# Performance work log

Hardware: AMD Instinct MI355X
Metric: run time of the kernel (lower is better)

Reference implementation:

```python
import jax, jax.numpy as jnp
import numpy as np

N = 8192      # nodes (= hidden_channels / heads)
E = 262144    # edges (avg degree 32)
IN = 256      # in_channels
H = 8         # heads
C = 32        # out_channels per head
NEG_SLOPE = 0.2


def setup_inputs() -> dict:
    key = jax.random.key(0)
    ks = jax.random.split(key, 8)
    x = jax.random.normal(ks[0], (N, IN), jnp.float32)
    edge_index = jax.random.randint(ks[1], (2, E), 0, N, dtype=jnp.int32)
    lin_w = jax.random.normal(ks[2], (H * C, IN), jnp.float32) * (1.0 / np.sqrt(IN))
    att_src = jax.random.normal(ks[3], (H, C), jnp.float32) * 0.1
    att_dst = jax.random.normal(ks[4], (H, C), jnp.float32) * 0.1
    bias = jax.random.normal(ks[5], (H * C,), jnp.float32) * 0.01
    out_w = jax.random.normal(ks[6], (C, N * H * C), jnp.float32) * (1.0 / np.sqrt(N * H * C))
    out_b = jax.random.normal(ks[7], (C,), jnp.float32) * 0.01
    return {"x": x, "edge_index": edge_index, "lin_w": lin_w, "att_src": att_src,
            "att_dst": att_dst, "bias": bias, "out_w": out_w, "out_b": out_b}


def reference(x, edge_index, lin_w, att_src, att_dst, bias, out_w, out_b):
    n = x.shape[0]
    # PyG GATConv default: add self loops
    loop = jnp.arange(n, dtype=edge_index.dtype)
    src = jnp.concatenate([edge_index[0], loop])  # message sources j
    dst = jnp.concatenate([edge_index[1], loop])  # message targets i
    # per-head linear projection: [n, H, C]
    xh = (x @ lin_w.T).reshape(n, H, C)
    a_src = jnp.einsum('nhc,hc->nh', xh, att_src)  # [n, H]
    a_dst = jnp.einsum('nhc,hc->nh', xh, att_dst)  # [n, H]
    # edge attention logits + segment softmax over incoming edges of each dst
    e = jax.nn.leaky_relu(a_src[src] + a_dst[dst], negative_slope=NEG_SLOPE)  # [E', H]
    m = jax.ops.segment_max(e, dst, num_segments=n)        # [n, H]
    ex = jnp.exp(e - m[dst])
    denom = jax.ops.segment_sum(ex, dst, num_segments=n)   # [n, H]
    alpha = ex / denom[dst]                                 # [E', H]
    # weighted scatter-add aggregation
    agg = jax.ops.segment_sum(alpha[:, :, None] * xh[src], dst, num_segments=n)  # [n, H, C]
    out = agg.reshape(n, H * C) + bias
    # flatten all nodes, dense output layer, softmax
    y = out.reshape(-1) @ out_w.T + out_b  # [C]
    return jax.nn.softmax(y)
```

## Files before the change

kernel.cpp:

```cpp
#include <hip/hip_runtime.h>


namespace {
constexpr int  kN    = 8192;
constexpr int  kE    = 262144;
constexpr int  kTotE = kE + kN;
constexpr long kK    = 2097152;
constexpr int  kNBF  = 2048;
}

__global__ __launch_bounds__(256) void gemm_xh(const float* __restrict__ x,
                                               const float* __restrict__ lw,
                                               float* __restrict__ xh) {
  __shared__ float As[16][68];
  __shared__ float Bs[16][68];
  const int t  = threadIdx.x;
  const int tx = t & 15, ty = t >> 4;
  const int rowBase = blockIdx.x * 64;
  const int colBase = blockIdx.y * 64;
  const int lr = t >> 2;
  const int lk = (t & 3) * 4;

  float acc[4][4] = {};
  for (int kc = 0; kc < 256; kc += 16) {
    float4 av = *(const float4*)(x  + (long)(rowBase + lr) * 256 + kc + lk);
    float4 bv = *(const float4*)(lw + (long)(colBase + lr) * 256 + kc + lk);
    __syncthreads();
    As[lk + 0][lr] = av.x; As[lk + 1][lr] = av.y; As[lk + 2][lr] = av.z; As[lk + 3][lr] = av.w;
    Bs[lk + 0][lr] = bv.x; Bs[lk + 1][lr] = bv.y; Bs[lk + 2][lr] = bv.z; Bs[lk + 3][lr] = bv.w;
    __syncthreads();
#pragma unroll
    for (int k = 0; k < 16; k++) {
      float4 a4 = *(const float4*)(&As[k][ty * 4]);
      float4 b4 = *(const float4*)(&Bs[k][tx * 4]);
      float aa[4] = {a4.x, a4.y, a4.z, a4.w};
      float bb[4] = {b4.x, b4.y, b4.z, b4.w};
#pragma unroll
      for (int i = 0; i < 4; i++)
#pragma unroll
        for (int j = 0; j < 4; j++) acc[i][j] += aa[i] * bb[j];
    }
  }
#pragma unroll
  for (int i = 0; i < 4; i++) {
    float4 o = make_float4(acc[i][0], acc[i][1], acc[i][2], acc[i][3]);
    *(float4*)(xh + (long)(rowBase + ty * 4 + i) * 256 + colBase + tx * 4) = o;
  }
}

__global__ __launch_bounds__(256) void att_cnt(const float* __restrict__ xh,
                                               const float* __restrict__ att_s,
                                               const float* __restrict__ att_d,
                                               float* __restrict__ a_src,
                                               float* __restrict__ a_dst,
                                               int* __restrict__ cnt) {
  const int n = blockIdx.x, t = threadIdx.x;
  float v = xh[(long)n * 256 + t];
  float s = v * att_s[t];
  float d = v * att_d[t];
#pragma unroll
  for (int off = 16; off; off >>= 1) {
    s += __shfl_down(s, off, 32);
    d += __shfl_down(d, off, 32);
  }
  if ((t & 31) == 0) {
    a_src[n * 8 + (t >> 5)] = s;
    a_dst[n * 8 + (t >> 5)] = d;
  }
  if (t == 0) cnt[n] = 1;
}

__global__ __launch_bounds__(256) void degree(const int* __restrict__ ei, int* __restrict__ cnt) {
  int idx = blockIdx.x * 256 + threadIdx.x;
  if (idx < kE) atomicAdd(&cnt[ei[kE + idx]], 1);
}

__global__ __launch_bounds__(1024) void scan_cnt(const int* __restrict__ cnt,
                                                 int* __restrict__ rowptr,
                                                 int* __restrict__ wpos) {
  __shared__ int s[1024];
  const int t = threadIdx.x;
  int v[8]; int sum = 0;
#pragma unroll
  for (int q = 0; q < 8; q++) { v[q] = cnt[t * 8 + q]; sum += v[q]; }
  s[t] = sum;
  __syncthreads();
  for (int off = 1; off < 1024; off <<= 1) {
    int add = (t >= off) ? s[t - off] : 0;
    __syncthreads();
    s[t] += add;
    __syncthreads();
  }
  int excl = s[t] - sum;
#pragma unroll
  for (int q = 0; q < 8; q++) {
    rowptr[t * 8 + q] = excl;
    wpos[t * 8 + q]   = excl;
    excl += v[q];
  }
  if (t == 1023) rowptr[kN] = s[1023];
}

__global__ __launch_bounds__(256) void scatter_csr(const int* __restrict__ ei,
                                                   const float* __restrict__ a_src,
                                                   const float* __restrict__ a_dst,
                                                   int* __restrict__ wpos,
                                                   int* __restrict__ csr,
                                                   float* __restrict__ w8) {
  int idx = blockIdx.x * 256 + threadIdx.x;
  if (idx >= kTotE) return;
  int s, d;
  if (idx < kE) { s = ei[idx]; d = ei[kE + idx]; }
  else          { s = idx - kE; d = s; }
  int pos = atomicAdd(&wpos[d], 1);
  csr[pos] = s;
  float4 s0 = *(const float4*)(a_src + s * 8);
  float4 s1 = *(const float4*)(a_src + s * 8 + 4);
  float4 d0 = *(const float4*)(a_dst + d * 8);
  float4 d1 = *(const float4*)(a_dst + d * 8 + 4);
  float e[8] = {s0.x + d0.x, s0.y + d0.y, s0.z + d0.z, s0.w + d0.w,
                s1.x + d1.x, s1.y + d1.y, s1.z + d1.z, s1.w + d1.w};
  float w[8];
#pragma unroll
  for (int h = 0; h < 8; h++) {
    float ee = (e[h] > 0.f) ? e[h] : 0.2f * e[h];
    w[h] = __expf(ee);
  }
  float4* wp = (float4*)(w8 + (long)pos * 8);
  wp[0] = make_float4(w[0], w[1], w[2], w[3]);
  wp[1] = make_float4(w[4], w[5], w[6], w[7]);
}

__global__ __launch_bounds__(256) void agg_kernel(const float* __restrict__ xh,
                                                  const float* __restrict__ w8,
                                                  const int* __restrict__ rowptr,
                                                  const int* __restrict__ csr,
                                                  const float* __restrict__ bias,
                                                  float* __restrict__ out_flat) {
  const int i = blockIdx.x, t = threadIdx.x, h = t >> 5;
  const int beg = rowptr[i], end = rowptr[i + 1];
  float acc = 0.f, den = 0.f;
  int j = beg;
  for (; j + 4 <= end; j += 4) {
    int s0 = csr[j], s1 = csr[j + 1], s2 = csr[j + 2], s3 = csr[j + 3];
    float w0 = w8[(long)(j + 0) * 8 + h];
    float w1 = w8[(long)(j + 1) * 8 + h];
    float w2 = w8[(long)(j + 2) * 8 + h];
    float w3 = w8[(long)(j + 3) * 8 + h];
    float f0 = xh[(long)s0 * 256 + t];
    float f1 = xh[(long)s1 * 256 + t];
    float f2 = xh[(long)s2 * 256 + t];
    float f3 = xh[(long)s3 * 256 + t];
    den += (w0 + w1) + (w2 + w3);
    acc += w0 * f0;
    acc += w1 * f1;
    acc += w2 * f2;
    acc += w3 * f3;
  }
  for (; j < end; j++) {
    int s = csr[j];
    float w = w8[(long)j * 8 + h];
    den += w;
    acc += w * xh[(long)s * 256 + t];
  }
  out_flat[(long)i * 256 + t] = acc / den + bias[t];
}

__global__ __launch_bounds__(256) void final_dot(const float* __restrict__ of,
                                                 const float* __restrict__ w,
                                                 float* __restrict__ part) {
  const int t = threadIdx.x, b = blockIdx.x;
  const long k = (long)b * 1024 + t * 4;
  float4 f = *(const float4*)(of + k);
  float acc[32];
#pragma unroll
  for (int c = 0; c < 32; c++) {
    float4 wv = *(const float4*)(w + (long)c * kK + k);
    acc[c] = wv.x * f.x + wv.y * f.y + wv.z * f.z + wv.w * f.w;
  }
#pragma unroll
  for (int c = 0; c < 32; c++) {
    float v = acc[c];
    v += __shfl_down(v, 32, 64);
    v += __shfl_down(v, 16, 64);
    v += __shfl_down(v, 8, 64);
    v += __shfl_down(v, 4, 64);
    v += __shfl_down(v, 2, 64);
    v += __shfl_down(v, 1, 64);
    acc[c] = v;
  }
  __shared__ float s[4][32];
  const int lane = t & 63, wid = t >> 6;
  if (lane == 0) {
#pragma unroll
    for (int c = 0; c < 32; c++) s[wid][c] = acc[c];
  }
  __syncthreads();
  if (t < 32) part[b * 32 + t] = s[0][t] + s[1][t] + s[2][t] + s[3][t];
}

__global__ __launch_bounds__(1024) void finalize(const float* __restrict__ part,
                                                 const float* __restrict__ ob,
                                                 float* __restrict__ out) {
  __shared__ float s[32][33];
  const int t = threadIdx.x;
  const int c = t & 31, r = t >> 5;
  float sum = 0.f;
  for (int i = r; i < kNBF; i += 32) sum += part[i * 32 + c];
  s[c][r] = sum;
  __syncthreads();
  if (t < 32) {
    float y = ob[t];
#pragma unroll
    for (int r2 = 0; r2 < 32; r2++) y += s[t][r2];
    float m = y;
#pragma unroll
    for (int off = 16; off; off >>= 1) m = fmaxf(m, __shfl_xor(m, off, 32));
    float e = __expf(y - m);
    float d = e;
#pragma unroll
    for (int off = 16; off; off >>= 1) d += __shfl_xor(d, off, 32);
    out[t] = e / d;
  }
}

extern "C" void kernel_launch(void* const* d_in, const int* in_sizes, int n_in,
                              void* d_out, int out_size, void* d_ws, size_t ws_size,
                              hipStream_t stream) {
  (void)in_sizes; (void)n_in; (void)out_size; (void)ws_size;
  const float* x     = (const float*)d_in[0];
  const int*   ei    = (const int*)  d_in[1];
  const float* lin_w = (const float*)d_in[2];
  const float* att_s = (const float*)d_in[3];
  const float* att_d = (const float*)d_in[4];
  const float* bias  = (const float*)d_in[5];
  const float* out_w = (const float*)d_in[6];
  const float* out_b = (const float*)d_in[7];
  float* out = (float*)d_out;

  float* xh       = (float*)d_ws;
  float* out_flat = xh + kK;
  float* a_src    = out_flat + kK;
  float* a_dst    = a_src + kN * 8;
  float* part     = a_dst + kN * 8;
  float* w8       = part + (long)kNBF * 32;
  int*   cnt      = (int*)(w8 + (long)kTotE * 8);
  int*   rowptr   = cnt + kN;
  int*   wpos     = rowptr + (kN + 1);
  int*   csr      = wpos + kN;

  gemm_xh    <<<dim3(128, 4), 256, 0, stream>>>(x, lin_w, xh);
  att_cnt    <<<kN, 256, 0, stream>>>(xh, att_s, att_d, a_src, a_dst, cnt);
  degree     <<<kE / 256, 256, 0, stream>>>(ei, cnt);
  scan_cnt   <<<1, 1024, 0, stream>>>(cnt, rowptr, wpos);
  scatter_csr<<<(kTotE + 255) / 256, 256, 0, stream>>>(ei, a_src, a_dst, wpos, csr, w8);
  agg_kernel <<<kN, 256, 0, stream>>>(xh, w8, rowptr, csr, bias, out_flat);
  final_dot  <<<kNBF, 256, 0, stream>>>(out_flat, out_w, part);
  finalize   <<<1, 1024, 0, stream>>>(part, out_b, out);
}
```

Measured before the change: 493.8 us.

## Use bf16 features for aggregation, fuse degree into attention kernel, nontemporal weight loads

The GEMM now also writes a bf16 copy of the projected features, and the aggregation kernel gathers those bf16 values with an unroll of 8 instead of 4, halving gather bytes. The degree count is folded into the attention kernel after a memset, with the self-loop +1 added during the scan. The final dot product loads the large output weight matrix with nontemporal loads to avoid polluting cache. The bf16 gather reduces precision of the aggregated features, and the GEMM gains an extra store.

```diff
diff --git a/kernel.cpp b/kernel.cpp
--- a/kernel.cpp
+++ b/kernel.cpp
@@ -9,9 +9,20 @@
 constexpr int  kNBF  = 2048;
 }
 
+typedef float vfloat4 __attribute__((ext_vector_type(4)));
+
+static __device__ __forceinline__ ushort f2bf(float f) {
+  unsigned u = __float_as_uint(f);
+  return (ushort)((u + 0x7FFFu + ((u >> 16) & 1u)) >> 16);
+}
+static __device__ __forceinline__ float bf2f(ushort b) {
+  return __uint_as_float(((unsigned)b) << 16);
+}
+
 __global__ __launch_bounds__(256) void gemm_xh(const float* __restrict__ x,
                                                const float* __restrict__ lw,
-                                               float* __restrict__ xh) {
+                                               float* __restrict__ xh,
+                                               ushort* __restrict__ xh_bf) {
   __shared__ float As[16][68];
   __shared__ float Bs[16][68];
   const int t  = threadIdx.x;
@@ -43,14 +54,18 @@
   }
 #pragma unroll
   for (int i = 0; i < 4; i++) {
+    const long row = rowBase + ty * 4 + i;
     float4 o = make_float4(acc[i][0], acc[i][1], acc[i][2], acc[i][3]);
-    *(float4*)(xh + (long)(rowBase + ty * 4 + i) * 256 + colBase + tx * 4) = o;
-  }
-}
-
-__global__ __launch_bounds__(256) void att_cnt(const float* __restrict__ xh,
+    *(float4*)(xh + row * 256 + colBase + tx * 4) = o;
+    ushort4 ob = make_ushort4(f2bf(o.x), f2bf(o.y), f2bf(o.z), f2bf(o.w));
+    *(ushort4*)(xh_bf + row * 256 + colBase + tx * 4) = ob;
+  }
+}
+
+__global__ __launch_bounds__(256) void att_deg(const float* __restrict__ xh,
                                                const float* __restrict__ att_s,
                                                const float* __restrict__ att_d,
+                                               const int* __restrict__ ei,
                                                float* __restrict__ a_src,
                                                float* __restrict__ a_dst,
                                                int* __restrict__ cnt) {
@@ -67,12 +82,8 @@
     a_src[n * 8 + (t >> 5)] = s;
     a_dst[n * 8 + (t >> 5)] = d;
   }
-  if (t == 0) cnt[n] = 1;
-}
-
-__global__ __launch_bounds__(256) void degree(const int* __restrict__ ei, int* __restrict__ cnt) {
-  int idx = blockIdx.x * 256 + threadIdx.x;
-  if (idx < kE) atomicAdd(&cnt[ei[kE + idx]], 1);
+  const int gid = n * 256 + t;
+  if (gid < kE) atomicAdd(&cnt[ei[kE + gid]], 1);
 }
 
 __global__ __launch_bounds__(1024) void scan_cnt(const int* __restrict__ cnt,
@@ -82,7 +93,7 @@
   const int t = threadIdx.x;
   int v[8]; int sum = 0;
 #pragma unroll
-  for (int q = 0; q < 8; q++) { v[q] = cnt[t * 8 + q]; sum += v[q]; }
+  for (int q = 0; q < 8; q++) { v[q] = cnt[t * 8 + q] + 1; sum += v[q]; }
   s[t] = sum;
   __syncthreads();
   for (int off = 1; off < 1024; off <<= 1) {
@@ -131,7 +142,7 @@
   wp[1] = make_float4(w[4], w[5], w[6], w[7]);
 }
 
-__global__ __launch_bounds__(256) void agg_kernel(const float* __restrict__ xh,
+__global__ __launch_bounds__(256) void agg_kernel(const ushort* __restrict__ xb,
                                                   const float* __restrict__ w8,
                                                   const int* __restrict__ rowptr,
                                                   const int* __restrict__ csr,
@@ -141,27 +152,22 @@
   const int beg = rowptr[i], end = rowptr[i + 1];
   float acc = 0.f, den = 0.f;
   int j = beg;
-  for (; j + 4 <= end; j += 4) {
-    int s0 = csr[j], s1 = csr[j + 1], s2 = csr[j + 2], s3 = csr[j + 3];
-    float w0 = w8[(long)(j + 0) * 8 + h];
-    float w1 = w8[(long)(j + 1) * 8 + h];
-    float w2 = w8[(long)(j + 2) * 8 + h];
-    float w3 = w8[(long)(j + 3) * 8 + h];
-    float f0 = xh[(long)s0 * 256 + t];
-    float f1 = xh[(long)s1 * 256 + t];
-    float f2 = xh[(long)s2 * 256 + t];
-    float f3 = xh[(long)s3 * 256 + t];
-    den += (w0 + w1) + (w2 + w3);
-    acc += w0 * f0;
-    acc += w1 * f1;
-    acc += w2 * f2;
-    acc += w3 * f3;
+  for (; j + 8 <= end; j += 8) {
+    int   s[8]; float w[8]; float f[8];
+#pragma unroll
+    for (int q = 0; q < 8; q++) s[q] = csr[j + q];
+#pragma unroll
+    for (int q = 0; q < 8; q++) w[q] = w8[(long)(j + q) * 8 + h];
+#pragma unroll
+    for (int q = 0; q < 8; q++) f[q] = bf2f(xb[(long)s[q] * 256 + t]);
+#pragma unroll
+    for (int q = 0; q < 8; q++) { den += w[q]; acc += w[q] * f[q]; }
   }
   for (; j < end; j++) {
-    int s = csr[j];
-    float w = w8[(long)j * 8 + h];
-    den += w;
-    acc += w * xh[(long)s * 256 + t];
+    int s0 = csr[j];
+    float w0 = w8[(long)j * 8 + h];
+    den += w0;
+    acc += w0 * bf2f(xb[(long)s0 * 256 + t]);
   }
   out_flat[(long)i * 256 + t] = acc / den + bias[t];
 }
@@ -175,7 +181,7 @@
   float acc[32];
 #pragma unroll
   for (int c = 0; c < 32; c++) {
-    float4 wv = *(const float4*)(w + (long)c * kK + k);
+    vfloat4 wv = __builtin_nontemporal_load((const vfloat4*)(w + (long)c * kK + k));
     acc[c] = wv.x * f.x + wv.y * f.y + wv.z * f.z + wv.w * f.w;
   }
 #pragma unroll
@@ -238,23 +244,24 @@
   const float* out_b = (const float*)d_in[7];
   float* out = (float*)d_out;
 
-  float* xh       = (float*)d_ws;
-  float* out_flat = xh + kK;
-  float* a_src    = out_flat + kK;
-  float* a_dst    = a_src + kN * 8;
-  float* part     = a_dst + kN * 8;
-  float* w8       = part + (long)kNBF * 32;
-  int*   cnt      = (int*)(w8 + (long)kTotE * 8);
-  int*   rowptr   = cnt + kN;
-  int*   wpos     = rowptr + (kN + 1);
-  int*   csr      = wpos + kN;
-
-  gemm_xh    <<<dim3(128, 4), 256, 0, stream>>>(x, lin_w, xh);
-  att_cnt    <<<kN, 256, 0, stream>>>(xh, att_s, att_d, a_src, a_dst, cnt);
-  degree     <<<kE / 256, 256, 0, stream>>>(ei, cnt);
+  float*  xh       = (float*)d_ws;
+  float*  out_flat = xh + kK;
+  float*  a_src    = out_flat + kK;
+  float*  a_dst    = a_src + kN * 8;
+  float*  part     = a_dst + kN * 8;
+  float*  w8       = part + (long)kNBF * 32;
+  ushort* xh_bf    = (ushort*)(w8 + (long)kTotE * 8);
+  int*    cnt      = (int*)(xh_bf + kK);
+  int*    rowptr   = cnt + kN;
+  int*    wpos     = rowptr + (kN + 1);
+  int*    csr      = wpos + kN;
+
+  (void)hipMemsetAsync(cnt, 0, kN * sizeof(int), stream);
+  gemm_xh    <<<dim3(128, 4), 256, 0, stream>>>(x, lin_w, xh, xh_bf);
+  att_deg    <<<kN, 256, 0, stream>>>(xh, att_s, att_d, ei, a_src, a_dst, cnt);
   scan_cnt   <<<1, 1024, 0, stream>>>(cnt, rowptr, wpos);
   scatter_csr<<<(kTotE + 255) / 256, 256, 0, stream>>>(ei, a_src, a_dst, wpos, csr, w8);
-  agg_kernel <<<kN, 256, 0, stream>>>(xh, w8, rowptr, csr, bias, out_flat);
+  agg_kernel <<<kN, 256, 0, stream>>>(xh_bf, w8, rowptr, csr, bias, out_flat);
   final_dot  <<<kNBF, 256, 0, stream>>>(out_flat, out_w, part);
   finalize   <<<1, 1024, 0, stream>>>(part, out_b, out);
 }
```

Measured after the change: 458.2 us. 1.08x faster.
